# Kernel optimization log

Measured on AMD Instinct MI355X. Metric: run time of the kernel, lower is better.

## Reference

```python
import jax, jax.numpy as jnp
import numpy as np

NUM_HEADS = 16
WINDOW = 256  # window_size: each query i attends to keys [max(0, i-W+1), i]


def setup_inputs() -> dict:
    key = jax.random.key(0)
    k1, k2, k3, k4, k5 = jax.random.split(key, 5)
    B, S, D = 2, 4096, 1024
    scale = 0.02
    return {
        "x": jax.random.normal(k1, (B, S, D), dtype=jnp.float32),
        "wq": jax.random.normal(k2, (D, D), dtype=jnp.float32) * scale,
        "wk": jax.random.normal(k3, (D, D), dtype=jnp.float32) * scale,
        "wv": jax.random.normal(k4, (D, D), dtype=jnp.float32) * scale,
        "wo": jax.random.normal(k5, (D, D), dtype=jnp.float32) * scale,
    }


def _sliding_window_attn(x, wq, wk, wv, wo):
    B, S, D = x.shape
    H, W = NUM_HEADS, WINDOW
    Dh = D // H
    nb = S // W  # number of query blocks (S assumed divisible by W)

    def proj(w):
        # nn.Linear: y = x @ w.T ; -> [B, H, nb, W, Dh]
        y = (x @ w.T).reshape(B, nb, W, H, Dh)
        return y.transpose(0, 3, 1, 2, 4)

    q = proj(wq)
    k = proj(wk)
    v = proj(wv)

    # Each query block j attends to key blocks j-1 and j (banded causal window).
    zpad = jnp.zeros((B, H, 1, W, Dh), dtype=x.dtype)
    kpad = jnp.concatenate([zpad, k], axis=2)  # [B,H,nb+1,W,Dh]
    vpad = jnp.concatenate([zpad, v], axis=2)
    k2 = jnp.concatenate([kpad[:, :, :-1], kpad[:, :, 1:]], axis=3)  # [B,H,nb,2W,Dh]
    v2 = jnp.concatenate([vpad[:, :, :-1], vpad[:, :, 1:]], axis=3)

    scores = jnp.einsum("bhjqd,bhjkd->bhjqk", q, k2) / jnp.sqrt(
        jnp.asarray(Dh, dtype=x.dtype)
    )  # [B,H,nb,W,2W]

    # Mask: query global pos i = j*W + qi; key global pos kp = (j-1)*W + ki.
    # Valid iff i-W+1 <= kp <= i  <=>  qi+1 <= ki <= qi+W ; and kp >= 0.
    qi = jnp.arange(W)[:, None]          # [W,1]
    ki = jnp.arange(2 * W)[None, :]      # [1,2W]
    band = (ki >= qi + 1) & (ki <= qi + W)                      # [W,2W]
    kpos_ok = (jnp.arange(nb)[:, None, None] - 1) * W + ki[None] >= 0  # [nb,1,2W]
    mask = band[None] & kpos_ok          # [nb,W,2W]

    neg = jnp.finfo(scores.dtype).min
    scores = jnp.where(mask[None, None], scores, neg)
    attn = jax.nn.softmax(scores, axis=-1)

    out = jnp.einsum("bhjqk,bhjkd->bhjqd", attn, v2)  # [B,H,nb,W,Dh]
    out = out.transpose(0, 2, 3, 1, 4).reshape(B, S, D)
    return out @ wo.T


def reference(x, wq, wk, wv, wo):
    return _sliding_window_attn(x, wq, wk, wv, wo)
```

## Files before the change

### kernel.cpp

```cpp
#include <hip/hip_runtime.h>

#define S_LEN 4096
#define DMODEL 1024
#define NH 16
#define DH 64
#define WIN 256
#define NQKV 3072

typedef __attribute__((ext_vector_type(8))) short short8;
typedef __attribute__((ext_vector_type(4))) short sh4;
typedef __attribute__((ext_vector_type(4))) float floatx4;

__device__ __forceinline__ ushort f2bf(float f) {
    union { float f; unsigned int i; } x;
    x.f = f;
    unsigned int r = x.i + 0x7FFFu + ((x.i >> 16) & 1u);
    return (ushort)(r >> 16);
}

__global__ __launch_bounds__(256) void cvt_all(const float* __restrict__ x,
                                               const float* __restrict__ wq,
                                               const float* __restrict__ wk,
                                               const float* __restrict__ wv,
                                               const float* __restrict__ wo,
                                               ushort* __restrict__ xb,
                                               ushort* __restrict__ W3b,
                                               ushort* __restrict__ wob,
                                               int nx8, int nw8) {
    int i = blockIdx.x * 256 + threadIdx.x;
    const float* src;
    ushort* dst;
    if (i < nx8) {
        src = x + (size_t)i * 8;            dst = xb + (size_t)i * 8;
    } else {
        int j = i - nx8;
        int which = j / nw8, r = j - which * nw8;
        if (which >= 4) return;
        const float* w4[4] = {wq, wk, wv, wo};
        src = w4[which] + (size_t)r * 8;
        dst = (which == 3 ? wob : W3b + (size_t)which * nw8 * 8) + (size_t)r * 8;
    }
    floatx4 f0 = *(const floatx4*)src;
    floatx4 f1 = *(const floatx4*)(src + 4);
    short8 v;
#pragma unroll
    for (int e = 0; e < 4; ++e) v[e] = (short)f2bf(f0[e]);
#pragma unroll
    for (int e = 0; e < 4; ++e) v[4 + e] = (short)f2bf(f1[e]);
    *(short8*)dst = v;
}

template <bool OUTF32>
__global__ __launch_bounds__(256) void gemm_bf16(const ushort* __restrict__ A,
                                                 const ushort* __restrict__ W,
                                                 void* __restrict__ Cout,
                                                 int M, int N, int K) {
    __shared__ __align__(16) ushort As[128 * 32];
    __shared__ __align__(16) ushort Ws[128 * 32];

    const int tid = threadIdx.x;
    const int w = tid >> 6, l = tid & 63;
    const int bm0 = blockIdx.y * 128, bn0 = blockIdx.x * 128;
    const int wm = (w >> 1) * 64, wn = (w & 1) * 64;
    const int lm = l & 15, quad = l >> 4;

    floatx4 acc[4][4] = {};

    const int row0 = tid >> 2, col0 = (tid & 3) * 8;
    const ushort* a0 = A + (size_t)(bm0 + row0) * K + col0;
    const ushort* a1 = A + (size_t)(bm0 + row0 + 64) * K + col0;
    const ushort* w0 = W + (size_t)(bn0 + row0) * K + col0;
    const ushort* w1 = W + (size_t)(bn0 + row0 + 64) * K + col0;

    for (int k0 = 0; k0 < K; k0 += 32) {
        __builtin_amdgcn_global_load_lds(
            (const __attribute__((address_space(1))) void*)(a0 + k0),
            (__attribute__((address_space(3))) void*)(As + tid * 8), 16, 0, 0);
        __builtin_amdgcn_global_load_lds(
            (const __attribute__((address_space(1))) void*)(a1 + k0),
            (__attribute__((address_space(3))) void*)(As + 2048 + tid * 8), 16, 0, 0);
        __builtin_amdgcn_global_load_lds(
            (const __attribute__((address_space(1))) void*)(w0 + k0),
            (__attribute__((address_space(3))) void*)(Ws + tid * 8), 16, 0, 0);
        __builtin_amdgcn_global_load_lds(
            (const __attribute__((address_space(1))) void*)(w1 + k0),
            (__attribute__((address_space(3))) void*)(Ws + 2048 + tid * 8), 16, 0, 0);
        __syncthreads();

        short8 af[4], wf[4];
#pragma unroll
        for (int mi = 0; mi < 4; ++mi)
            af[mi] = *(const short8*)&As[(wm + mi * 16 + lm) * 32 + quad * 8];
#pragma unroll
        for (int ni = 0; ni < 4; ++ni)
            wf[ni] = *(const short8*)&Ws[(wn + ni * 16 + lm) * 32 + quad * 8];
#pragma unroll
        for (int mi = 0; mi < 4; ++mi)
#pragma unroll
            for (int ni = 0; ni < 4; ++ni)
                acc[mi][ni] = __builtin_amdgcn_mfma_f32_16x16x32_bf16(
                    af[mi], wf[ni], acc[mi][ni], 0, 0, 0);
        __syncthreads();
    }

#pragma unroll
    for (int mi = 0; mi < 4; ++mi)
#pragma unroll
        for (int ni = 0; ni < 4; ++ni)
#pragma unroll
            for (int r = 0; r < 4; ++r) {
                int row = bm0 + wm + mi * 16 + quad * 4 + r;
                int col = bn0 + wn + ni * 16 + lm;
                if (OUTF32)
                    ((float*)Cout)[(size_t)row * N + col] = acc[mi][ni][r];
                else
                    ((ushort*)Cout)[(size_t)row * N + col] = f2bf(acc[mi][ni][r]);
            }
}

template <bool OUTF32>
__global__ __launch_bounds__(256, 2) void gemm_qkv(const ushort* __restrict__ A,
                                                   const ushort* __restrict__ W,
                                                   void* __restrict__ Cout,
                                                   int M, int N, int K) {
    __shared__ __align__(16) ushort As[128 * 64];
    __shared__ __align__(16) ushort Ws[256 * 64];

    const int tid = threadIdx.x;
    const int w = tid >> 6, l = tid & 63;
    const int bm0 = blockIdx.y * 128, bn0 = blockIdx.x * 256;
    const int wm = (w >> 1) * 64, wn = (w & 1) * 128;
    const int lm = l & 15, quad = l >> 4;

    floatx4 acc[4][8] = {};

    int arow[4], acol[4];
#pragma unroll
    for (int p = 0; p < 4; ++p) {
        int c = p * 256 + tid;
        arow[p] = c >> 3;
        acol[p] = (((c & 7) ^ (arow[p] & 7))) * 8;
    }
    int wrow[8], wcol[8];
#pragma unroll
    for (int p = 0; p < 8; ++p) {
        int c = p * 256 + tid;
        wrow[p] = c >> 3;
        wcol[p] = (((c & 7) ^ (wrow[p] & 7))) * 8;
    }

    for (int k0 = 0; k0 < K; k0 += 64) {
#pragma unroll
        for (int p = 0; p < 4; ++p)
            __builtin_amdgcn_global_load_lds(
                (const __attribute__((address_space(1))) void*)
                    (A + (size_t)(bm0 + arow[p]) * K + k0 + acol[p]),
                (__attribute__((address_space(3))) void*)(As + p * 2048 + tid * 8),
                16, 0, 0);
#pragma unroll
        for (int p = 0; p < 8; ++p)
            __builtin_amdgcn_global_load_lds(
                (const __attribute__((address_space(1))) void*)
                    (W + (size_t)(bn0 + wrow[p]) * K + k0 + wcol[p]),
                (__attribute__((address_space(3))) void*)(Ws + p * 2048 + tid * 8),
                16, 0, 0);
        __syncthreads();

#pragma unroll
        for (int kk = 0; kk < 2; ++kk) {
            const int sseg = ((kk * 4 + quad) ^ (lm & 7)) * 8;
            short8 af[4], wf[8];
#pragma unroll
            for (int mi = 0; mi < 4; ++mi)
                af[mi] = *(const short8*)&As[(wm + mi * 16 + lm) * 64 + sseg];
#pragma unroll
            for (int ni = 0; ni < 8; ++ni)
                wf[ni] = *(const short8*)&Ws[(wn + ni * 16 + lm) * 64 + sseg];
#pragma unroll
            for (int mi = 0; mi < 4; ++mi)
#pragma unroll
                for (int ni = 0; ni < 8; ++ni)
                    acc[mi][ni] = __builtin_amdgcn_mfma_f32_16x16x32_bf16(
                        af[mi], wf[ni], acc[mi][ni], 0, 0, 0);
        }
        __syncthreads();
    }

#pragma unroll
    for (int mi = 0; mi < 4; ++mi)
#pragma unroll
        for (int ni = 0; ni < 8; ++ni)
#pragma unroll
            for (int r = 0; r < 4; ++r) {
                int row = bm0 + wm + mi * 16 + quad * 4 + r;
                int col = bn0 + wn + ni * 16 + lm;
                if (OUTF32)
                    ((float*)Cout)[(size_t)row * N + col] = acc[mi][ni][r];
                else
                    ((ushort*)Cout)[(size_t)row * N + col] = f2bf(acc[mi][ni][r]);
            }
}

#define KSP 72
#define VTP 136
#define PSP 40

__global__ __launch_bounds__(256) void swattn_mfma(const ushort* __restrict__ QKV,
                                                   ushort* __restrict__ O) {
    __shared__ __align__(16) ushort Ks[128 * KSP];
    __shared__ __align__(16) ushort Vt[64 * VTP];
    __shared__ __align__(16) ushort Ps[2][4 * 64 * PSP];
    __shared__ __align__(16) float lW[256];

    const int j = blockIdx.x, h = blockIdx.y, b = blockIdx.z;
    const int tid = threadIdx.x;
    const int w = tid >> 6, l = tid & 63;
    const int quad = l >> 4, lc = l & 15;

    const size_t base = (size_t)b * S_LEN * NQKV + (size_t)h * DH;
    const ushort* Qp = QKV + base;
    const ushort* Kp = QKV + base + DMODEL;
    const ushort* Vp = QKV + base + 2 * DMODEL;

    short8 qf[4][2];
#pragma unroll
    for (int nq = 0; nq < 4; ++nq)
#pragma unroll
        for (int kk = 0; kk < 2; ++kk)
            qf[nq][kk] = *(const short8*)(Qp +
                (size_t)(j * 256 + w * 64 + nq * 16 + lc) * NQKV + kk * 32 + quad * 8);

    floatx4 o[4][4] = {};
    float lsum[4] = {0.f, 0.f, 0.f, 0.f};

    const float sscale = 0.18033688011112042f;
    const float M0 = 2.0f;
    const int qlo = w * 64, qhi = w * 64 + 63;

    for (int c = 0; c < 4; ++c) {
        const int kg0 = (j - 1) * 256 + c * 128;
        if (kg0 < 0) continue;
        __syncthreads();
#pragma unroll
        for (int i = 0; i < 4; ++i) {
            int cc = i * 256 + tid, key = cc >> 3, seg = cc & 7;
            *(short8*)&Ks[key * KSP + seg * 8] =
                *(const short8*)(Kp + (size_t)(kg0 + key) * NQKV + seg * 8);
            short8 vv = *(const short8*)(Vp + (size_t)(kg0 + key) * NQKV + seg * 8);
#pragma unroll
            for (int e = 0; e < 8; ++e)
                Vt[(e * 8 + seg) * VTP + key] = (ushort)vv[e];
        }
        __syncthreads();

        const int krel0 = c * 128 - 256;
#pragma unroll
        for (int g = 0; g < 4; ++g) {
            const int k0 = krel0 + g * 32;
            if (k0 > qhi || k0 + 31 < qlo - 255) continue;
            ushort* Pw = &Ps[g & 1][w * 64 * PSP];

            floatx4 st[2][4];
            const floatx4 zero = {};
#pragma unroll
            for (int kt = 0; kt < 2; ++kt) {
                short8 kf0 = *(const short8*)&Ks[(g * 32 + kt * 16 + lc) * KSP + quad * 8];
                short8 kf1 = *(const short8*)&Ks[(g * 32 + kt * 16 + lc) * KSP + 32 + quad * 8];
#pragma unroll
                for (int nq = 0; nq < 4; ++nq) {
                    int kmin = k0 + kt * 16, qmin = qlo + nq * 16;
                    if (kmin > qmin + 15 || kmin + 270 < qmin) {
                        st[kt][nq] = zero;
                        continue;
                    }
                    st[kt][nq] = __builtin_amdgcn_mfma_f32_16x16x32_bf16(kf0, qf[nq][0], zero, 0, 0, 0);
                    st[kt][nq] = __builtin_amdgcn_mfma_f32_16x16x32_bf16(kf1, qf[nq][1], st[kt][nq], 0, 0, 0);
                }
            }
#pragma unroll
            for (int kt = 0; kt < 2; ++kt)
#pragma unroll
                for (int nq = 0; nq < 4; ++nq) {
                    sh4 pv;
                    int kmin = k0 + kt * 16, qmin = qlo + nq * 16;
                    if (kmin > qmin + 15 || kmin + 270 < qmin) {
                        pv[0] = pv[1] = pv[2] = pv[3] = 0;
                    } else if (kmin + 15 <= qmin && kmin + 240 >= qmin) {
#pragma unroll
                        for (int r = 0; r < 4; ++r) {
                            float p = exp2f(st[kt][nq][r] * sscale - M0);
                            lsum[nq] += p;
                            pv[r] = (short)f2bf(p);
                        }
                    } else {
#pragma unroll
                        for (int r = 0; r < 4; ++r) {
                            int krel = kmin + quad * 4 + r;
                            int qrel = qmin + lc;
                            bool valid = (krel <= qrel) && (krel + 255 >= qrel);
                            float p = valid ? exp2f(st[kt][nq][r] * sscale - M0) : 0.f;
                            lsum[nq] += p;
                            pv[r] = (short)f2bf(p);
                        }
                    }
                    *(sh4*)&Pw[(nq * 16 + lc) * PSP + kt * 16 + quad * 4] = pv;
                }
            __threadfence_block();

            short8 vf[4];
#pragma unroll
            for (int nd = 0; nd < 4; ++nd) {
                int prow = (lc & 7) * 8 + nd * 2 + (lc >> 3);
                vf[nd] = *(const short8*)&Vt[prow * VTP + g * 32 + quad * 8];
            }
#pragma unroll
            for (int mq = 0; mq < 4; ++mq) {
                int qmin = qlo + mq * 16;
                if (k0 > qmin + 15 || k0 + 286 < qmin) continue;
                short8 pf = *(const short8*)&Pw[(mq * 16 + lc) * PSP + quad * 8];
#pragma unroll
                for (int nd = 0; nd < 4; ++nd)
                    o[mq][nd] = __builtin_amdgcn_mfma_f32_16x16x32_bf16(pf, vf[nd], o[mq][nd], 0, 0, 0);
            }
        }
    }

#pragma unroll
    for (int nq = 0; nq < 4; ++nq) {
        lsum[nq] += __shfl_xor(lsum[nq], 16);
        lsum[nq] += __shfl_xor(lsum[nq], 32);
    }
    if (l < 16) {
#pragma unroll
        for (int nq = 0; nq < 4; ++nq) lW[w * 64 + nq * 16 + l] = lsum[nq];
    }
    __threadfence_block();
#pragma unroll
    for (int mq = 0; mq < 4; ++mq) {
        floatx4 lv = *(const floatx4*)&lW[w * 64 + mq * 16 + quad * 4];
#pragma unroll
        for (int r = 0; r < 4; ++r) {
            float inv = 1.f / lv[r];
            int token = j * 256 + w * 64 + mq * 16 + quad * 4 + r;
#pragma unroll
            for (int nd = 0; nd < 4; ++nd)
                O[(size_t)b * S_LEN * DMODEL + (size_t)token * DMODEL + h * DH + nd * 16 + lc] =
                    f2bf(o[mq][nd][r] * inv);
        }
    }
}

extern "C" void kernel_launch(void* const* d_in, const int* in_sizes, int n_in,
                              void* d_out, int out_size, void* d_ws, size_t ws_size,
                              hipStream_t stream) {
    const float* x  = (const float*)d_in[0];
    const float* wq = (const float*)d_in[1];
    const float* wk = (const float*)d_in[2];
    const float* wv = (const float*)d_in[3];
    const float* wo = (const float*)d_in[4];
    float* out = (float*)d_out;

    const int D = DMODEL;
    const int M = in_sizes[0] / D;
    const int Bb = M / S_LEN;

    ushort* xb   = (ushort*)d_ws;
    ushort* W3b  = xb + (size_t)M * D;
    ushort* wob  = W3b + (size_t)NQKV * D;
    ushort* QKVb = wob + (size_t)D * D;
    ushort* Ob   = xb;

    const int nx8 = M * D / 8, nw8 = D * D / 8;
    const int ntot = nx8 + 4 * nw8;
    cvt_all<<<dim3((ntot + 255) / 256), dim3(256), 0, stream>>>(
        x, wq, wk, wv, wo, xb, W3b, wob, nx8, nw8);

    gemm_qkv<false><<<dim3(NQKV / 256, M / 128), dim3(256), 0, stream>>>(
        xb, W3b, QKVb, M, NQKV, D);

    swattn_mfma<<<dim3(S_LEN / WIN, NH, Bb), dim3(256), 0, stream>>>(QKVb, Ob);

    gemm_bf16<true><<<dim3(D / 128, M / 128), dim3(256), 0, stream>>>(
        Ob, wob, out, M, D, D);
}
```

Baseline: 229.0 us.

## Unify GEMMs into triple-buffered pipelined kernel with XCD-aware tile remapping

Both projection GEMMs are replaced by one templated kernel that triple-buffers the LDS tiles. Each K-step issues the async global-to-LDS loads two steps ahead and waits with vmcnt counters, so only one barrier sits on each step. It also remaps block indices so neighbouring row tiles land on the same XCD for better L2 reuse, and it uses a new rotation swizzle on the LDS layout to avoid bank conflicts. The K tile shrinks to 32 and LDS use rises, which risks lower occupancy and makes the hand-written waitcnt values fragile.

```diff
diff --git a/kernel.cpp b/kernel.cpp
--- a/kernel.cpp
+++ b/kernel.cpp
@@ -50,151 +50,119 @@
     *(short8*)dst = v;
 }
 
-template <bool OUTF32>
-__global__ __launch_bounds__(256) void gemm_bf16(const ushort* __restrict__ A,
-                                                 const ushort* __restrict__ W,
-                                                 void* __restrict__ Cout,
-                                                 int M, int N, int K) {
-    __shared__ __align__(16) ushort As[128 * 32];
-    __shared__ __align__(16) ushort Ws[128 * 32];
+template <int NF, bool OUTF32>
+__global__ __launch_bounds__(256, 2) void gemm_2ph(const ushort* __restrict__ A,
+                                                   const ushort* __restrict__ W,
+                                                   void* __restrict__ Cout,
+                                                   int M, int N, int K) {
+    constexpr int BN = NF * 32;
+    constexpr int WCH = BN / 64;
+    __shared__ __align__(16) ushort As[3][128 * 32];
+    __shared__ __align__(16) ushort Ws[3][BN * 32];
 
     const int tid = threadIdx.x;
     const int w = tid >> 6, l = tid & 63;
-    const int bm0 = blockIdx.y * 128, bn0 = blockIdx.x * 128;
-    const int wm = (w >> 1) * 64, wn = (w & 1) * 64;
     const int lm = l & 15, quad = l >> 4;
 
-    floatx4 acc[4][4] = {};
-
-    const int row0 = tid >> 2, col0 = (tid & 3) * 8;
-    const ushort* a0 = A + (size_t)(bm0 + row0) * K + col0;
-    const ushort* a1 = A + (size_t)(bm0 + row0 + 64) * K + col0;
-    const ushort* w0 = W + (size_t)(bn0 + row0) * K + col0;
-    const ushort* w1 = W + (size_t)(bn0 + row0 + 64) * K + col0;
-
-    for (int k0 = 0; k0 < K; k0 += 32) {
-        __builtin_amdgcn_global_load_lds(
-            (const __attribute__((address_space(1))) void*)(a0 + k0),
-            (__attribute__((address_space(3))) void*)(As + tid * 8), 16, 0, 0);
-        __builtin_amdgcn_global_load_lds(
-            (const __attribute__((address_space(1))) void*)(a1 + k0),
-            (__attribute__((address_space(3))) void*)(As + 2048 + tid * 8), 16, 0, 0);
-        __builtin_amdgcn_global_load_lds(
-            (const __attribute__((address_space(1))) void*)(w0 + k0),
-            (__attribute__((address_space(3))) void*)(Ws + tid * 8), 16, 0, 0);
-        __builtin_amdgcn_global_load_lds(
-            (const __attribute__((address_space(1))) void*)(w1 + k0),
-            (__attribute__((address_space(3))) void*)(Ws + 2048 + tid * 8), 16, 0, 0);
-        __syncthreads();
-
-        short8 af[4], wf[4];
+    int bx, by;
+    {
+        const int nbx = gridDim.x, nby = gridDim.y;
+        if ((nby & 7) == 0) {
+            const int lin = blockIdx.y * nbx + blockIdx.x;
+            const int rpb = nby >> 3;
+            const int xcd = lin & 7, idx = lin >> 3;
+            bx = idx / rpb;
+            by = xcd * rpb + (idx - bx * rpb);
+        } else {
+            bx = blockIdx.x;
+            by = blockIdx.y;
+        }
+    }
+    const int bm0 = by * 128, bn0 = bx * BN;
+    const int wm = (w >> 1) * 64, wn = (w & 1) * (BN / 2);
+
+    const ushort* Ag = A + (size_t)bm0 * K;
+    const ushort* Wg = W + (size_t)bn0 * K;
+    int aoff[2];
+#pragma unroll
+    for (int p = 0; p < 2; ++p) {
+        int n = p * 256 + tid, r = n >> 2, s = n & 3;
+        int ks = (s - (((r & 3) + ((r >> 2) & 3)) & 3)) & 3;
+        aoff[p] = r * K + ks * 8;
+    }
+    int woff[WCH];
+#pragma unroll
+    for (int p = 0; p < WCH; ++p) {
+        int n = p * 256 + tid, r = n >> 2, s = n & 3;
+        int ks = (s - (((r & 3) + ((r >> 2) & 3)) & 3)) & 3;
+        woff[p] = r * K + ks * 8;
+    }
+
+    auto stage = [&](int bf, int k0) {
+        ushort* ad = &As[bf][tid * 8];
+        ushort* wd = &Ws[bf][tid * 8];
+#pragma unroll
+        for (int p = 0; p < 2; ++p)
+            __builtin_amdgcn_global_load_lds(
+                (const __attribute__((address_space(1))) void*)(Ag + aoff[p] + k0),
+                (__attribute__((address_space(3))) void*)(ad + p * 2048), 16, 0, 0);
+#pragma unroll
+        for (int p = 0; p < WCH; ++p)
+            __builtin_amdgcn_global_load_lds(
+                (const __attribute__((address_space(1))) void*)(Wg + woff[p] + k0),
+                (__attribute__((address_space(3))) void*)(wd + p * 2048), 16, 0, 0);
+    };
+
+    floatx4 acc[4][NF] = {};
+    const int fs = ((quad + (lm & 3) + ((lm >> 2) & 3)) & 3) * 8;
+
+    const int nt = K >> 5;
+    stage(0, 0);
+    stage(1, 32);
+    if constexpr (NF == 8) asm volatile("s_waitcnt vmcnt(6)" ::: "memory");
+    else                   asm volatile("s_waitcnt vmcnt(4)" ::: "memory");
+    __builtin_amdgcn_s_barrier();
+
+    int rb = 0, sb = 2;
+    for (int t = 0; t < nt; ++t) {
+        if (t + 2 < nt) stage(sb, (t + 2) << 5);
+        const ushort* Ac = As[rb];
+        const ushort* Wc = Ws[rb];
+        short8 af[4], wf[NF];
 #pragma unroll
         for (int mi = 0; mi < 4; ++mi)
-            af[mi] = *(const short8*)&As[(wm + mi * 16 + lm) * 32 + quad * 8];
-#pragma unroll
-        for (int ni = 0; ni < 4; ++ni)
-            wf[ni] = *(const short8*)&Ws[(wn + ni * 16 + lm) * 32 + quad * 8];
+            af[mi] = *(const short8*)&Ac[(wm + mi * 16 + lm) * 32 + fs];
+#pragma unroll
+        for (int ni = 0; ni < NF; ++ni)
+            wf[ni] = *(const short8*)&Wc[(wn + ni * 16 + lm) * 32 + fs];
 #pragma unroll
         for (int mi = 0; mi < 4; ++mi)
 #pragma unroll
-            for (int ni = 0; ni < 4; ++ni)
+            for (int ni = 0; ni < NF; ++ni)
                 acc[mi][ni] = __builtin_amdgcn_mfma_f32_16x16x32_bf16(
                     af[mi], wf[ni], acc[mi][ni], 0, 0, 0);
-        __syncthreads();
+        if (t + 2 < nt) {
+            if constexpr (NF == 8)
+                asm volatile("s_waitcnt vmcnt(6) lgkmcnt(0)" ::: "memory");
+            else
+                asm volatile("s_waitcnt vmcnt(4) lgkmcnt(0)" ::: "memory");
+        } else {
+            asm volatile("s_waitcnt vmcnt(0) lgkmcnt(0)" ::: "memory");
+        }
+        __builtin_amdgcn_s_barrier();
+        rb = (rb == 2) ? 0 : rb + 1;
+        sb = (sb == 2) ? 0 : sb + 1;
     }
 
 #pragma unroll
     for (int mi = 0; mi < 4; ++mi)
 #pragma unroll
-        for (int ni = 0; ni < 4; ++ni)
+        for (int ni = 0; ni < NF; ++ni)
 #pragma unroll
             for (int r = 0; r < 4; ++r) {
                 int row = bm0 + wm + mi * 16 + quad * 4 + r;
                 int col = bn0 + wn + ni * 16 + lm;
-                if (OUTF32)
-                    ((float*)Cout)[(size_t)row * N + col] = acc[mi][ni][r];
-                else
-                    ((ushort*)Cout)[(size_t)row * N + col] = f2bf(acc[mi][ni][r]);
-            }
-}
-
-template <bool OUTF32>
-__global__ __launch_bounds__(256, 2) void gemm_qkv(const ushort* __restrict__ A,
-                                                   const ushort* __restrict__ W,
-                                                   void* __restrict__ Cout,
-                                                   int M, int N, int K) {
-    __shared__ __align__(16) ushort As[128 * 64];
-    __shared__ __align__(16) ushort Ws[256 * 64];
-
-    const int tid = threadIdx.x;
-    const int w = tid >> 6, l = tid & 63;
-    const int bm0 = blockIdx.y * 128, bn0 = blockIdx.x * 256;
-    const int wm = (w >> 1) * 64, wn = (w & 1) * 128;
-    const int lm = l & 15, quad = l >> 4;
-
-    floatx4 acc[4][8] = {};
-
-    int arow[4], acol[4];
-#pragma unroll
-    for (int p = 0; p < 4; ++p) {
-        int c = p * 256 + tid;
-        arow[p] = c >> 3;
-        acol[p] = (((c & 7) ^ (arow[p] & 7))) * 8;
-    }
-    int wrow[8], wcol[8];
-#pragma unroll
-    for (int p = 0; p < 8; ++p) {
-        int c = p * 256 + tid;
-        wrow[p] = c >> 3;
-        wcol[p] = (((c & 7) ^ (wrow[p] & 7))) * 8;
-    }
-
-    for (int k0 = 0; k0 < K; k0 += 64) {
-#pragma unroll
-        for (int p = 0; p < 4; ++p)
-            __builtin_amdgcn_global_load_lds(
-                (const __attribute__((address_space(1))) void*)
-                    (A + (size_t)(bm0 + arow[p]) * K + k0 + acol[p]),
-                (__attribute__((address_space(3))) void*)(As + p * 2048 + tid * 8),
-                16, 0, 0);
-#pragma unroll
-        for (int p = 0; p < 8; ++p)
-            __builtin_amdgcn_global_load_lds(
-                (const __attribute__((address_space(1))) void*)
-                    (W + (size_t)(bn0 + wrow[p]) * K + k0 + wcol[p]),
-                (__attribute__((address_space(3))) void*)(Ws + p * 2048 + tid * 8),
-                16, 0, 0);
-        __syncthreads();
-
-#pragma unroll
-        for (int kk = 0; kk < 2; ++kk) {
-            const int sseg = ((kk * 4 + quad) ^ (lm & 7)) * 8;
-            short8 af[4], wf[8];
-#pragma unroll
-            for (int mi = 0; mi < 4; ++mi)
-                af[mi] = *(const short8*)&As[(wm + mi * 16 + lm) * 64 + sseg];
-#pragma unroll
-            for (int ni = 0; ni < 8; ++ni)
-                wf[ni] = *(const short8*)&Ws[(wn + ni * 16 + lm) * 64 + sseg];
-#pragma unroll
-            for (int mi = 0; mi < 4; ++mi)
-#pragma unroll
-                for (int ni = 0; ni < 8; ++ni)
-                    acc[mi][ni] = __builtin_amdgcn_mfma_f32_16x16x32_bf16(
-                        af[mi], wf[ni], acc[mi][ni], 0, 0, 0);
-        }
-        __syncthreads();
-    }
-
-#pragma unroll
-    for (int mi = 0; mi < 4; ++mi)
-#pragma unroll
-        for (int ni = 0; ni < 8; ++ni)
-#pragma unroll
-            for (int r = 0; r < 4; ++r) {
-                int row = bm0 + wm + mi * 16 + quad * 4 + r;
-                int col = bn0 + wn + ni * 16 + lm;
-                if (OUTF32)
+                if constexpr (OUTF32)
                     ((float*)Cout)[(size_t)row * N + col] = acc[mi][ni][r];
                 else
                     ((ushort*)Cout)[(size_t)row * N + col] = f2bf(acc[mi][ni][r]);
@@ -375,11 +343,11 @@
     cvt_all<<<dim3((ntot + 255) / 256), dim3(256), 0, stream>>>(
         x, wq, wk, wv, wo, xb, W3b, wob, nx8, nw8);
 
-    gemm_qkv<false><<<dim3(NQKV / 256, M / 128), dim3(256), 0, stream>>>(
+    gemm_2ph<8, false><<<dim3(NQKV / 256, M / 128), dim3(256), 0, stream>>>(
         xb, W3b, QKVb, M, NQKV, D);
 
     swattn_mfma<<<dim3(S_LEN / WIN, NH, Bb), dim3(256), 0, stream>>>(QKVb, Ob);
 
-    gemm_bf16<true><<<dim3(D / 128, M / 128), dim3(256), 0, stream>>>(
+    gemm_2ph<4, true><<<dim3(D / 128, M / 128), dim3(256), 0, stream>>>(
         Ob, wob, out, M, D, D);
 }
```

Result: slower. 240.8 us (+5.2%).

## Add double-buffered 256x256 QKV GEMM and reuse 128x256 kernel for output projection

Applied to the files above, without the earlier changes.

Replaces the QKV projection GEMM with a new 512-thread, 256x256-tile kernel. It double-buffers LDS and splits each K-step into four quarter MFMA phases, interleaving async global-to-LDS loads with explicit vmcnt waits, barriers and s_setprio. The output projection now uses the former 128x256 QKV kernel instead of the small 128x128 one with K-step 32. Both kernels also remap block indices so that blocks sharing an XCD work on contiguous row bands, for better L2 reuse. In exchange, the hand-placed waitcnt/barrier schedule is fragile, and the larger tiles produce fewer blocks, which may leave CUs underused (QKV grid is 12x32 = 384 blocks).

```diff
diff --git a/kernel.cpp b/kernel.cpp
--- a/kernel.cpp
+++ b/kernel.cpp
@@ -50,85 +50,193 @@
     *(short8*)dst = v;
 }
 
+#define GLOAD16(src, dst)                                                     \
+    __builtin_amdgcn_global_load_lds(                                         \
+        (const __attribute__((address_space(1))) void*)(src),                 \
+        (__attribute__((address_space(3))) void*)(dst), 16, 0, 0)
+#define WAITV4 asm volatile("s_waitcnt vmcnt(4)" ::: "memory")
+#define WAITV2 asm volatile("s_waitcnt vmcnt(2)" ::: "memory")
+#define WAITV0 asm volatile("s_waitcnt vmcnt(0)" ::: "memory")
+#define BARR   asm volatile("s_barrier" ::: "memory")
+#define WAITL                                                                 \
+    do {                                                                      \
+        asm volatile("s_waitcnt lgkmcnt(0)" ::: "memory");                    \
+        __builtin_amdgcn_sched_barrier(0);                                    \
+    } while (0)
+
 template <bool OUTF32>
-__global__ __launch_bounds__(256) void gemm_bf16(const ushort* __restrict__ A,
-                                                 const ushort* __restrict__ W,
-                                                 void* __restrict__ Cout,
-                                                 int M, int N, int K) {
-    __shared__ __align__(16) ushort As[128 * 32];
-    __shared__ __align__(16) ushort Ws[128 * 32];
+__global__ __launch_bounds__(512, 2) void gemm256(const ushort* __restrict__ A,
+                                                  const ushort* __restrict__ W,
+                                                  void* __restrict__ Cout,
+                                                  int M, int N, int K) {
+    __shared__ __align__(16) ushort AS[2][2][128 * 64];
+    __shared__ __align__(16) ushort BS[2][2][128 * 64];
 
     const int tid = threadIdx.x;
     const int w = tid >> 6, l = tid & 63;
-    const int bm0 = blockIdx.y * 128, bn0 = blockIdx.x * 128;
-    const int wm = (w >> 1) * 64, wn = (w & 1) * 64;
-    const int lm = l & 15, quad = l >> 4;
-
-    floatx4 acc[4][4] = {};
-
-    const int row0 = tid >> 2, col0 = (tid & 3) * 8;
-    const ushort* a0 = A + (size_t)(bm0 + row0) * K + col0;
-    const ushort* a1 = A + (size_t)(bm0 + row0 + 64) * K + col0;
-    const ushort* w0 = W + (size_t)(bn0 + row0) * K + col0;
-    const ushort* w1 = W + (size_t)(bn0 + row0 + 64) * K + col0;
-
-    for (int k0 = 0; k0 < K; k0 += 32) {
-        __builtin_amdgcn_global_load_lds(
-            (const __attribute__((address_space(1))) void*)(a0 + k0),
-            (__attribute__((address_space(3))) void*)(As + tid * 8), 16, 0, 0);
-        __builtin_amdgcn_global_load_lds(
-            (const __attribute__((address_space(1))) void*)(a1 + k0),
-            (__attribute__((address_space(3))) void*)(As + 2048 + tid * 8), 16, 0, 0);
-        __builtin_amdgcn_global_load_lds(
-            (const __attribute__((address_space(1))) void*)(w0 + k0),
-            (__attribute__((address_space(3))) void*)(Ws + tid * 8), 16, 0, 0);
-        __builtin_amdgcn_global_load_lds(
-            (const __attribute__((address_space(1))) void*)(w1 + k0),
-            (__attribute__((address_space(3))) void*)(Ws + 2048 + tid * 8), 16, 0, 0);
-        __syncthreads();
-
-        short8 af[4], wf[4];
-#pragma unroll
-        for (int mi = 0; mi < 4; ++mi)
-            af[mi] = *(const short8*)&As[(wm + mi * 16 + lm) * 32 + quad * 8];
+    const int lm = l & 15, quad = l >> 4, l7 = l & 7;
+    const int mh = w >> 2;
+    const int wq = w & 3;
+
+    int bx, by;
+    {
+        const int nbx = gridDim.x, nby = gridDim.y;
+        if ((nby & 7) == 0) {
+            const int lin = blockIdx.y * nbx + blockIdx.x;
+            const int rpb = nby >> 3;
+            const int xcd = lin & 7, idx = lin >> 3;
+            bx = idx / rpb;
+            by = xcd * rpb + (idx - bx * rpb);
+        } else {
+            bx = blockIdx.x;
+            by = blockIdx.y;
+        }
+    }
+    const int bm0 = by * 256, bn0 = bx * 256;
+
+    const ushort* Ag = A + (size_t)bm0 * K;
+    const ushort* Wg = W + (size_t)bn0 * K;
+
+    int ksOff[2], aRowB[2], bRowB[2];
+#pragma unroll
+    for (int p = 0; p < 2; ++p) {
+        int c = p * 512 + tid, riu = c >> 3;
+        ksOff[p] = ((c & 7) ^ (riu & 7)) * 8;
+        aRowB[p] = (riu >> 6) * 128 + (riu & 63);
+        bRowB[p] = (riu >> 5) * 64 + (riu & 31);
+    }
+
+    auto stA = [&](int bf, int u, int k0) {
+#pragma unroll
+        for (int p = 0; p < 2; ++p)
+            GLOAD16(Ag + (size_t)(aRowB[p] + u * 64) * K + k0 + ksOff[p],
+                    &AS[bf][u][(p * 512 + tid) * 8]);
+    };
+    auto stB = [&](int bf, int u, int k0) {
+#pragma unroll
+        for (int p = 0; p < 2; ++p)
+            GLOAD16(Wg + (size_t)(bRowB[p] + u * 32) * K + k0 + ksOff[p],
+                    &BS[bf][u][(p * 512 + tid) * 8]);
+    };
+
+    const int s0 = (quad ^ l7) * 8;
+    const int s1 = ((4 + quad) ^ l7) * 8;
+
+    floatx4 acc[8][4] = {};
+    short8 aR[4][2], b0[2][2], b1[2][2];
+
+    auto rdA = [&](int bf, int g, short8(&r)[4][2]) {
+#pragma unroll
+        for (int m = 0; m < 4; ++m) {
+            const ushort* p = &AS[bf][g][(mh * 64 + m * 16 + lm) * 64];
+            r[m][0] = *(const short8*)(p + s0);
+            r[m][1] = *(const short8*)(p + s1);
+        }
+    };
+    auto rdB = [&](int bf, int g, short8(&r)[2][2]) {
+#pragma unroll
+        for (int n = 0; n < 2; ++n) {
+            const ushort* p = &BS[bf][g][(wq * 32 + n * 16 + lm) * 64];
+            r[n][0] = *(const short8*)(p + s0);
+            r[n][1] = *(const short8*)(p + s1);
+        }
+    };
+
+#define MMAQ(AF, BF_, GM, GN)                                                  \
+    do {                                                                       \
+        __builtin_amdgcn_s_setprio(1);                                         \
+        _Pragma("unroll") for (int m_ = 0; m_ < 4; ++m_)                       \
+            _Pragma("unroll") for (int n_ = 0; n_ < 2; ++n_) {                 \
+            acc[(GM)*4 + m_][(GN)*2 + n_] =                                    \
+                __builtin_amdgcn_mfma_f32_16x16x32_bf16(                       \
+                    AF[m_][0], BF_[n_][0], acc[(GM)*4 + m_][(GN)*2 + n_], 0,   \
+                    0, 0);                                                     \
+            acc[(GM)*4 + m_][(GN)*2 + n_] =                                    \
+                __builtin_amdgcn_mfma_f32_16x16x32_bf16(                       \
+                    AF[m_][1], BF_[n_][1], acc[(GM)*4 + m_][(GN)*2 + n_], 0,   \
+                    0, 0);                                                     \
+        }                                                                      \
+        __builtin_amdgcn_s_setprio(0);                                         \
+    } while (0)
+
+    stA(0, 0, 0);
+    stB(0, 0, 0);
+    stB(0, 1, 0);
+    stA(0, 1, 0);
+    WAITV4;
+    BARR;
+
+    const int nt = K >> 6;
+    for (int t = 0; t < nt; ++t) {
+        const int bf = t & 1, nb = bf ^ 1, kn = (t + 1) << 6;
+        const bool nl = (t + 1 < nt);
+        rdA(bf, 0, aR);
+        rdB(bf, 0, b0);
+        if (nl) { stA(nb, 0, kn); WAITV4; } else { WAITV2; }
+        BARR;
+        WAITL;
+        MMAQ(aR, b0, 0, 0);
+        BARR;
+        rdB(bf, 1, b1);
+        if (nl) { stB(nb, 0, kn); WAITV4; } else { WAITV0; }
+        BARR;
+        WAITL;
+        MMAQ(aR, b1, 0, 1);
+        BARR;
+        rdA(bf, 1, aR);
+        if (nl) stB(nb, 1, kn);
+        BARR;
+        WAITL;
+        MMAQ(aR, b1, 1, 1);
+        BARR;
+        if (nl) { stA(nb, 1, kn); WAITV4; }
+        BARR;
+        MMAQ(aR, b0, 1, 0);
+        BARR;
+    }
+
+#pragma unroll
+    for (int mi = 0; mi < 8; ++mi)
 #pragma unroll
         for (int ni = 0; ni < 4; ++ni)
-            wf[ni] = *(const short8*)&Ws[(wn + ni * 16 + lm) * 32 + quad * 8];
-#pragma unroll
-        for (int mi = 0; mi < 4; ++mi)
-#pragma unroll
-            for (int ni = 0; ni < 4; ++ni)
-                acc[mi][ni] = __builtin_amdgcn_mfma_f32_16x16x32_bf16(
-                    af[mi], wf[ni], acc[mi][ni], 0, 0, 0);
-        __syncthreads();
-    }
-
-#pragma unroll
-    for (int mi = 0; mi < 4; ++mi)
-#pragma unroll
-        for (int ni = 0; ni < 4; ++ni)
 #pragma unroll
             for (int r = 0; r < 4; ++r) {
-                int row = bm0 + wm + mi * 16 + quad * 4 + r;
-                int col = bn0 + wn + ni * 16 + lm;
-                if (OUTF32)
+                int row = bm0 + mh * 128 + mi * 16 + quad * 4 + r;
+                int col = bn0 + wq * 64 + ni * 16 + lm;
+                if constexpr (OUTF32)
                     ((float*)Cout)[(size_t)row * N + col] = acc[mi][ni][r];
                 else
                     ((ushort*)Cout)[(size_t)row * N + col] = f2bf(acc[mi][ni][r]);
             }
+#undef MMAQ
 }
 
 template <bool OUTF32>
-__global__ __launch_bounds__(256, 2) void gemm_qkv(const ushort* __restrict__ A,
-                                                   const ushort* __restrict__ W,
-                                                   void* __restrict__ Cout,
-                                                   int M, int N, int K) {
+__global__ __launch_bounds__(256, 2) void gemm128(const ushort* __restrict__ A,
+                                                  const ushort* __restrict__ W,
+                                                  void* __restrict__ Cout,
+                                                  int M, int N, int K) {
     __shared__ __align__(16) ushort As[128 * 64];
     __shared__ __align__(16) ushort Ws[256 * 64];
 
     const int tid = threadIdx.x;
     const int w = tid >> 6, l = tid & 63;
-    const int bm0 = blockIdx.y * 128, bn0 = blockIdx.x * 256;
+
+    int bx, by;
+    {
+        const int nbx = gridDim.x, nby = gridDim.y;
+        if ((nby & 7) == 0) {
+            const int lin = blockIdx.y * nbx + blockIdx.x;
+            const int rpb = nby >> 3;
+            const int xcd = lin & 7, idx = lin >> 3;
+            bx = idx / rpb;
+            by = xcd * rpb + (idx - bx * rpb);
+        } else {
+            bx = blockIdx.x;
+            by = blockIdx.y;
+        }
+    }
+    const int bm0 = by * 128, bn0 = bx * 256;
     const int wm = (w >> 1) * 64, wn = (w & 1) * 128;
     const int lm = l & 15, quad = l >> 4;
 
@@ -152,18 +260,12 @@
     for (int k0 = 0; k0 < K; k0 += 64) {
 #pragma unroll
         for (int p = 0; p < 4; ++p)
-            __builtin_amdgcn_global_load_lds(
-                (const __attribute__((address_space(1))) void*)
-                    (A + (size_t)(bm0 + arow[p]) * K + k0 + acol[p]),
-                (__attribute__((address_space(3))) void*)(As + p * 2048 + tid * 8),
-                16, 0, 0);
+            GLOAD16(A + (size_t)(bm0 + arow[p]) * K + k0 + acol[p],
+                    As + p * 2048 + tid * 8);
 #pragma unroll
         for (int p = 0; p < 8; ++p)
-            __builtin_amdgcn_global_load_lds(
-                (const __attribute__((address_space(1))) void*)
-                    (W + (size_t)(bn0 + wrow[p]) * K + k0 + wcol[p]),
-                (__attribute__((address_space(3))) void*)(Ws + p * 2048 + tid * 8),
-                16, 0, 0);
+            GLOAD16(W + (size_t)(bn0 + wrow[p]) * K + k0 + wcol[p],
+                    Ws + p * 2048 + tid * 8);
         __syncthreads();
 
 #pragma unroll
@@ -194,7 +296,7 @@
             for (int r = 0; r < 4; ++r) {
                 int row = bm0 + wm + mi * 16 + quad * 4 + r;
                 int col = bn0 + wn + ni * 16 + lm;
-                if (OUTF32)
+                if constexpr (OUTF32)
                     ((float*)Cout)[(size_t)row * N + col] = acc[mi][ni][r];
                 else
                     ((ushort*)Cout)[(size_t)row * N + col] = f2bf(acc[mi][ni][r]);
@@ -375,11 +477,11 @@
     cvt_all<<<dim3((ntot + 255) / 256), dim3(256), 0, stream>>>(
         x, wq, wk, wv, wo, xb, W3b, wob, nx8, nw8);
 
-    gemm_qkv<false><<<dim3(NQKV / 256, M / 128), dim3(256), 0, stream>>>(
+    gemm256<false><<<dim3(NQKV / 256, M / 256), dim3(512), 0, stream>>>(
         xb, W3b, QKVb, M, NQKV, D);
 
     swattn_mfma<<<dim3(S_LEN / WIN, NH, Bb), dim3(256), 0, stream>>>(QKVb, Ob);
 
-    gemm_bf16<true><<<dim3(D / 128, M / 128), dim3(256), 0, stream>>>(
+    gemm128<true><<<dim3(D / 256, M / 128), dim3(256), 0, stream>>>(
         Ob, wob, out, M, D, D);
 }
```

New measurement: 232.0 us. About the same (+1.3%).
